# Kernel optimization log

Hardware: AMD Instinct MI355X
Metric: run time of the kernel (lower is better)

The kernel has to match this reference:

```python
import jax, jax.numpy as jnp
import numpy as np

N, E = 50000, 1600000
DIN, DOUT, H, DG = 128, 128, 8, 64
DH = DOUT // H  # per-head dim
NEG_SLOPE = 0.2


def _leaky(x):
    return jnp.where(x >= 0, x, NEG_SLOPE * x)


def setup_inputs() -> dict:
    key = jax.random.key(0)
    ks = jax.random.split(key, 9)
    row = jax.random.randint(ks[0], (E,), 0, N, dtype=jnp.int32)
    col = jax.random.randint(ks[1], (E,), 0, N, dtype=jnp.int32)
    val = jax.random.uniform(ks[2], (E,), dtype=jnp.float32)  # normalized adj values
    feat = jax.random.normal(ks[3], (N, DIN), dtype=jnp.float32)
    W = jax.random.normal(ks[4], (2, H, DIN, DH), dtype=jnp.float32) * 0.05
    b = jnp.zeros((2, H, DH), dtype=jnp.float32)
    att = jax.random.normal(ks[5], (H, 2 * DH), dtype=jnp.float32) * 0.1
    offset = jnp.zeros((2, DOUT), dtype=jnp.float32)
    scale = jnp.ones((2, DOUT), dtype=jnp.float32)
    weight_gate = jax.random.normal(ks[6], (2 * DIN + DG, H), dtype=jnp.float32) * 0.05
    weight_pool_gate = jax.random.normal(ks[7], (DIN, DG), dtype=jnp.float32) * 0.05
    return {"row": row, "col": col, "val": val, "feat": feat, "W": W, "b": b,
            "att": att, "offset": offset, "scale": scale,
            "weight_gate": weight_gate, "weight_pool_gate": weight_pool_gate}


def reference(row, col, val, feat, W, b, att, offset, scale, weight_gate, weight_pool_gate):
    # ---- gate values (GaAN eq. 3) ----
    zj = feat @ weight_pool_gate                                   # [N, DG]
    zmax = jax.ops.segment_max(zj[col], row, num_segments=N)       # max-pool over neighbors
    zmax = jnp.where(jnp.isfinite(zmax), zmax, 0.0)                # isolated nodes -> 0
    nmean = jax.ops.segment_sum(val[:, None] * feat[col], row, num_segments=N)  # spmm(adj, feat)
    gate = jnp.concatenate([feat, zmax, nmean], axis=1) @ weight_gate            # [N, H]
    # ---- per-order, per-head linear + relu ----
    fp = jax.nn.relu(jnp.einsum('nd,ohdk->onhk', feat, W) + b[:, None])  # [2, N, H, DH]
    f0, f1 = fp[0], fp[1]                                          # self / neighbor feats
    # ---- attention-weighted sparse aggregation ----
    a_self = _leaky(jnp.einsum('nhk,hk->nh', f0, att[:, :DH]))     # [N, H]
    a_neigh = _leaky(jnp.einsum('nhk,hk->nh', f1, att[:, DH:]))    # [N, H]
    w_edge = (a_self[row] + a_neigh[col]) * val[:, None]           # [E, H]
    agg = jax.ops.segment_sum(w_edge[:, :, None] * f1[col], row, num_segments=N)  # [N, H, DH]
    agg = agg * gate[:, :, None]                                   # gated heads
    h0 = f0.reshape(N, DOUT)
    h1 = agg.reshape(N, DOUT)
    # ---- per-node norm (torch _batch_norm over feature dim) ----
    def norm(x, s, o):
        mu = jnp.mean(x, axis=1, keepdims=True)
        var = jnp.var(x, axis=1, keepdims=True) + 1e-9
        return (x - mu) * s * jax.lax.rsqrt(var) + o
    h0 = norm(h0, scale[0], offset[0])
    h1 = norm(h1, scale[1], offset[1])
    return h0 + h1  # aggr == 'mean'
```

## Files before the change

kernel.cpp:

```cpp
#include <hip/hip_runtime.h>
#include <hip/hip_bf16.h>
#include <math.h>

#define DIN   128
#define DOUTC 128
#define HH    8
#define DHH   16
#define DGG   64
#define NCOLS 336
#define NTILE 21
#define BSHIFT 7
#define CAP   6144
#define EPB   4096

typedef __attribute__((ext_vector_type(8))) short short8v;
typedef __attribute__((ext_vector_type(4))) float float4v;

__global__ void cvt_feat(const float* __restrict__ feat, __hip_bfloat16* __restrict__ featb, int total8) {
    int i = blockIdx.x * 256 + threadIdx.x;
    if (i < total8) {
        const float4* p = reinterpret_cast<const float4*>(feat) + 2 * (size_t)i;
        float4 x = p[0], y = p[1];
        union { __hip_bfloat16 h[8]; short8v v; } pk;
        pk.h[0] = __float2bfloat16(x.x); pk.h[1] = __float2bfloat16(x.y);
        pk.h[2] = __float2bfloat16(x.z); pk.h[3] = __float2bfloat16(x.w);
        pk.h[4] = __float2bfloat16(y.x); pk.h[5] = __float2bfloat16(y.y);
        pk.h[6] = __float2bfloat16(y.z); pk.h[7] = __float2bfloat16(y.w);
        reinterpret_cast<short8v*>(featb)[i] = pk.v;
    }
}

__global__ void prep2(const float* __restrict__ W, const float* __restrict__ b,
                      const float* __restrict__ Wg, const float* __restrict__ Wpg,
                      __hip_bfloat16* __restrict__ Btb, float* __restrict__ biasv) {
    int idx = blockIdx.x * 256 + threadIdx.x;
    if (idx < NCOLS * DIN) {
        int j = idx >> 7;
        int k = idx & 127;
        float v;
        if (j < 256) {
            int o = j >> 7, jj = j & 127, h = jj >> 4, kd = jj & 15;
            v = W[((o * HH + h) * DIN + k) * DHH + kd];
        } else if (j < 320) {
            v = Wpg[k * DGG + (j - 256)];
        } else if (j < 328) {
            v = Wg[k * HH + (j - 320)];
        } else {
            v = Wg[(192 + k) * HH + (j - 328)];
        }
        Btb[idx] = __float2bfloat16(v);
    }
    if (idx < NCOLS) {
        float bv = 0.f;
        if (idx < 256) { int o = idx >> 7, jj = idx & 127; bv = b[(o * HH + (jj >> 4)) * DHH + (jj & 15)]; }
        biasv[idx] = bv;
    }
}

__global__ __launch_bounds__(256, 2) void dense_mfma(
    const __hip_bfloat16* __restrict__ featb, const __hip_bfloat16* __restrict__ Btb,
    const float* __restrict__ biasv,
    float* __restrict__ f0, __hip_bfloat16* __restrict__ f1b, __hip_bfloat16* __restrict__ zjb,
    float* __restrict__ fg0, float* __restrict__ nodedat, int N) {
    int t   = threadIdx.x;
    int wid = t >> 6, l = t & 63;
    int r0  = blockIdx.x * 128 + wid * 32;
    int lr  = l & 15;
    int lk  = l >> 4;

    short8v a[2][4];
    #pragma unroll
    for (int rt = 0; rt < 2; ++rt) {
        int node = r0 + rt * 16 + lr;
        if (node >= N) node = N - 1;
        const short8v* ap = reinterpret_cast<const short8v*>(&featb[(size_t)node * DIN + lk * 8]);
        #pragma unroll
        for (int kk = 0; kk < 4; ++kk) a[rt][kk] = ap[kk * 4];
    }

    float4v acc[2][NTILE];
    #pragma unroll
    for (int rt = 0; rt < 2; ++rt)
        #pragma unroll
        for (int n = 0; n < NTILE; ++n) acc[rt][n] = (float4v)0.f;

    const short8v* bp = reinterpret_cast<const short8v*>(Btb) + (lr * 16 + lk);
    #pragma unroll
    for (int n = 0; n < NTILE; ++n) {
        #pragma unroll
        for (int kk = 0; kk < 4; ++kk) {
            short8v bv = bp[n * 256 + kk * 4];
            acc[0][n] = __builtin_amdgcn_mfma_f32_16x16x32_bf16(a[0][kk], bv, acc[0][n], 0, 0, 0);
            acc[1][n] = __builtin_amdgcn_mfma_f32_16x16x32_bf16(a[1][kk], bv, acc[1][n], 0, 0, 0);
        }
    }

    #pragma unroll
    for (int rt = 0; rt < 2; ++rt) {
        #pragma unroll
        for (int rg = 0; rg < 4; ++rg) {
            int node = r0 + rt * 16 + lk * 4 + rg;
            if (node < N) {
                #pragma unroll
                for (int n = 0; n < NTILE; ++n) {
                    int col = n * 16 + lr;
                    float v = acc[rt][n][rg] + biasv[col];
                    if (n < 8) {
                        v = v > 0.f ? v : 0.f;
                        f0[(size_t)node * DOUTC + col] = v;
                    } else if (n < 16) {
                        v = v > 0.f ? v : 0.f;
                        f1b[(size_t)node * DOUTC + (col - 128)] = __float2bfloat16(v);
                    } else if (n < 20) {
                        zjb[(size_t)node * DGG + (col - 256)] = __float2bfloat16(v);
                    } else {
                        if (lr < 8) fg0[node * HH + lr] = v;
                        else        nodedat[(size_t)node * 16 + 8 + (lr - 8)] = v;
                    }
                }
            }
        }
    }
}

__global__ void attn_kernel(const float* __restrict__ f0, const __hip_bfloat16* __restrict__ f1b,
                            const float* __restrict__ att,
                            float* __restrict__ a_self, float* __restrict__ nodedat, int N) {
    int g = blockIdx.x * 256 + threadIdx.x;
    if (g >= N * 16) return;
    int node = g >> 4, u = g & 15, h = u >> 1;
    float s = 0.f;
    if ((u & 1) == 0) {
        const float4* p  = reinterpret_cast<const float4*>(&f0[(size_t)node * DOUTC + h * DHH]);
        const float*  av = &att[h * 32];
        #pragma unroll
        for (int q = 0; q < 4; ++q) {
            float4 x = p[q];
            s = fmaf(x.x, av[q * 4 + 0], fmaf(x.y, av[q * 4 + 1],
                fmaf(x.z, av[q * 4 + 2], fmaf(x.w, av[q * 4 + 3], s))));
        }
        s = (s >= 0.f) ? s : 0.2f * s;
        a_self[node * HH + h] = s;
    } else {
        const short8v* p = reinterpret_cast<const short8v*>(&f1b[(size_t)node * DOUTC + h * DHH]);
        const float*  av = &att[h * 32 + DHH];
        union { short8v v; __hip_bfloat16 hh[8]; } pk0, pk1;
        pk0.v = p[0]; pk1.v = p[1];
        #pragma unroll
        for (int q = 0; q < 8; ++q) s = fmaf(__bfloat162float(pk0.hh[q]), av[q], s);
        #pragma unroll
        for (int q = 0; q < 8; ++q) s = fmaf(__bfloat162float(pk1.hh[q]), av[8 + q], s);
        s = (s >= 0.f) ? s : 0.2f * s;
        nodedat[(size_t)node * 16 + h] = s;
    }
}

__global__ __launch_bounds__(256) void bhist(const int* __restrict__ row, int* __restrict__ gHist, int E) {
    __shared__ int hist[512];
    int tid = threadIdx.x;
    hist[tid] = 0; hist[tid + 256] = 0;
    __syncthreads();
    int e0 = blockIdx.x * EPB;
    #pragma unroll
    for (int k = 0; k < 16; ++k) {
        int e = e0 + k * 256 + tid;
        if (e < E) atomicAdd(&hist[row[e] >> BSHIFT], 1);
    }
    __syncthreads();
    if (hist[tid])       atomicAdd(&gHist[tid], hist[tid]);
    if (hist[tid + 256]) atomicAdd(&gHist[tid + 256], hist[tid + 256]);
}

__global__ __launch_bounds__(512) void bscan(const int* __restrict__ gHist, int* __restrict__ gBase,
                                             int* __restrict__ gCursor, int nbuck) {
    __shared__ int s[512];
    int tid = threadIdx.x;
    s[tid] = (tid < nbuck) ? gHist[tid] : 0;
    __syncthreads();
    for (int off = 1; off < 512; off <<= 1) {
        int add = (tid >= off) ? s[tid - off] : 0;
        __syncthreads();
        s[tid] += add;
        __syncthreads();
    }
    if (tid < nbuck) {
        int excl = (tid == 0) ? 0 : s[tid - 1];
        gBase[tid] = excl;
        gCursor[tid] = excl;
    }
}

__global__ __launch_bounds__(256) void bscatter(const int* __restrict__ row, const int* __restrict__ col,
                                                const float* __restrict__ val, int* __restrict__ gCursor,
                                                int2* __restrict__ ebuf, int E) {
    __shared__ int hist[512], base[512], rank[512];
    int tid = threadIdx.x;
    hist[tid] = 0; hist[tid + 256] = 0;
    __syncthreads();
    int e0 = blockIdx.x * EPB;
    #pragma unroll
    for (int k = 0; k < 16; ++k) {
        int e = e0 + k * 256 + tid;
        if (e < E) atomicAdd(&hist[row[e] >> BSHIFT], 1);
    }
    __syncthreads();
    if (hist[tid])       base[tid] = atomicAdd(&gCursor[tid], hist[tid]);
    if (hist[tid + 256]) base[tid + 256] = atomicAdd(&gCursor[tid + 256], hist[tid + 256]);
    rank[tid] = 0; rank[tid + 256] = 0;
    __syncthreads();
    #pragma unroll
    for (int k = 0; k < 16; ++k) {
        int e = e0 + k * 256 + tid;
        if (e < E) {
            int r = row[e];
            int bk = r >> BSHIFT;
            int loc = atomicAdd(&rank[bk], 1);
            int2 pk;
            pk.x = col[e] | ((r & 127) << 16);
            pk.y = __float_as_int(val[e]);
            ebuf[base[bk] + loc] = pk;
        }
    }
}

__global__ __launch_bounds__(256) void bsort(const int2* __restrict__ ebuf, const int* __restrict__ gHist,
                                             const int* __restrict__ gBase, int2* __restrict__ efin,
                                             int* __restrict__ rowptr, int N) {
    __shared__ int2 ent[CAP];
    __shared__ int h0[128], sc[128], rk[128];
    int b = blockIdx.x, tid = threadIdx.x;
    int cnt = gHist[b]; if (cnt > CAP) cnt = CAP;
    int base = gBase[b];
    if (tid < 128) h0[tid] = 0;
    __syncthreads();
    for (int i = tid; i < cnt; i += 256) {
        int2 e = ebuf[base + i];
        ent[i] = e;
        atomicAdd(&h0[(e.x >> 16) & 127], 1);
    }
    __syncthreads();
    if (tid < 128) sc[tid] = h0[tid];
    __syncthreads();
    for (int off = 1; off < 128; off <<= 1) {
        int add = (tid < 128 && tid >= off) ? sc[tid - off] : 0;
        __syncthreads();
        if (tid < 128) sc[tid] += add;
        __syncthreads();
    }
    if (tid < 128) {
        int excl = sc[tid] - h0[tid];
        rk[tid] = excl;
        int grow = b * 128 + tid;
        if (grow <= N) rowptr[grow] = base + excl;
    }
    __syncthreads();
    for (int i = tid; i < cnt; i += 256) {
        int2 e = ent[i];
        int dst = base + atomicAdd(&rk[(e.x >> 16) & 127], 1);
        efin[dst] = e;
    }
}

#define UN 8
__global__ __launch_bounds__(128) void edge_kernel(
    const int* __restrict__ rowptr, const int2* __restrict__ ef,
    const __hip_bfloat16* __restrict__ f1b, const __hip_bfloat16* __restrict__ zjb,
    const float* __restrict__ a_self, const float* __restrict__ nodedat,
    const float* __restrict__ fg0, const float* __restrict__ Wg,
    const float* __restrict__ f0, const float* __restrict__ scale, const float* __restrict__ offset,
    float* __restrict__ out) {
    int r = blockIdx.x;
    int t = threadIdx.x;
    int start = rowptr[r], end = rowptr[r + 1];

    __shared__ float lds_z[64];
    __shared__ float lds_n8[8];
    __shared__ float lds_gate[8];

    float accA0 = 0.f, accA1 = 0.f, accZ = -INFINITY, accN8 = 0.f;
    int h = t >> 3;
    float asr = 0.f;
    if (t < 64) asr = a_self[r * HH + h];
    int j = t - 64;

    int i = start;
    for (; i + UN <= end; i += UN) {
        int   c[UN]; float v[UN];
        #pragma unroll
        for (int u = 0; u < UN; ++u) {
            int2 eu = ef[i + u];
            c[u] = eu.x & 0xFFFF;
            v[u] = __int_as_float(eu.y);
        }
        if (t < 64) {
            float an[UN];
            #pragma unroll
            for (int u = 0; u < UN; ++u) an[u] = nodedat[(size_t)c[u] * 16 + h];
            __hip_bfloat162 f2[UN];
            #pragma unroll
            for (int u = 0; u < UN; ++u)
                f2[u] = *reinterpret_cast<const __hip_bfloat162*>(&f1b[(size_t)c[u] * DOUTC + 2 * t]);
            #pragma unroll
            for (int u = 0; u < UN; ++u) {
                float w = (asr + an[u]) * v[u];
                accA0 = fmaf(w, __bfloat162float(f2[u].x), accA0);
                accA1 = fmaf(w, __bfloat162float(f2[u].y), accA1);
            }
        } else {
            float z[UN];
            #pragma unroll
            for (int u = 0; u < UN; ++u) z[u] = __bfloat162float(zjb[(size_t)c[u] * DGG + j]);
            #pragma unroll
            for (int u = 0; u < UN; ++u) accZ = fmaxf(accZ, z[u]);
            if (j < 8) {
                float g2[UN];
                #pragma unroll
                for (int u = 0; u < UN; ++u) g2[u] = nodedat[(size_t)c[u] * 16 + 8 + j];
                #pragma unroll
                for (int u = 0; u < UN; ++u) accN8 = fmaf(v[u], g2[u], accN8);
            }
        }
    }
    for (; i < end; ++i) {
        int2 eu = ef[i];
        int   c = eu.x & 0xFFFF;
        float v = __int_as_float(eu.y);
        if (t < 64) {
            float w = (asr + nodedat[(size_t)c * 16 + h]) * v;
            __hip_bfloat162 f2 = *reinterpret_cast<const __hip_bfloat162*>(&f1b[(size_t)c * DOUTC + 2 * t]);
            accA0 = fmaf(w, __bfloat162float(f2.x), accA0);
            accA1 = fmaf(w, __bfloat162float(f2.y), accA1);
        } else {
            accZ = fmaxf(accZ, __bfloat162float(zjb[(size_t)c * DGG + j]));
            if (j < 8) accN8 = fmaf(v, nodedat[(size_t)c * 16 + 8 + j], accN8);
        }
    }

    if (t >= 64) {
        lds_z[j] = (end > start) ? accZ : 0.f;
        if (j < 8) lds_n8[j] = accN8;
    }
    __syncthreads();

    if (t < 8) {
        float g = fg0[r * HH + t] + lds_n8[t];
        #pragma unroll
        for (int k = 0; k < 64; ++k) g = fmaf(lds_z[k], Wg[(128 + k) * HH + t], g);
        lds_gate[t] = g;
    }
    __syncthreads();

    if (t < 64) {
        float gh  = lds_gate[h];
        float h1x = accA0 * gh, h1y = accA1 * gh;
        float2 f0v = *reinterpret_cast<const float2*>(&f0[r * DOUTC + 2 * t]);
        float s0  = f0v.x + f0v.y;
        float s0q = f0v.x * f0v.x + f0v.y * f0v.y;
        float s1  = h1x + h1y;
        float s1q = h1x * h1x + h1y * h1y;
        #pragma unroll
        for (int off = 32; off > 0; off >>= 1) {
            s0  += __shfl_xor(s0,  off);
            s0q += __shfl_xor(s0q, off);
            s1  += __shfl_xor(s1,  off);
            s1q += __shfl_xor(s1q, off);
        }
        float mu0  = s0 * (1.f / 128.f), mu1 = s1 * (1.f / 128.f);
        float rs0  = rsqrtf(s0q * (1.f / 128.f) - mu0 * mu0 + 1e-9f);
        float rs1  = rsqrtf(s1q * (1.f / 128.f) - mu1 * mu1 + 1e-9f);
        float2 sc0 = *reinterpret_cast<const float2*>(&scale[2 * t]);
        float2 sc1 = *reinterpret_cast<const float2*>(&scale[128 + 2 * t]);
        float2 of0 = *reinterpret_cast<const float2*>(&offset[2 * t]);
        float2 of1 = *reinterpret_cast<const float2*>(&offset[128 + 2 * t]);
        float2 o2;
        o2.x = (f0v.x - mu0) * sc0.x * rs0 + of0.x + (h1x - mu1) * sc1.x * rs1 + of1.x;
        o2.y = (f0v.y - mu0) * sc0.y * rs0 + of0.y + (h1y - mu1) * sc1.y * rs1 + of1.y;
        *reinterpret_cast<float2*>(&out[r * DOUTC + 2 * t]) = o2;
    }
}

extern "C" void kernel_launch(void* const* d_in, const int* in_sizes, int n_in,
                              void* d_out, int out_size, void* d_ws, size_t ws_size,
                              hipStream_t stream) {
    const int*   row  = (const int*)  d_in[0];
    const int*   col  = (const int*)  d_in[1];
    const float* val  = (const float*)d_in[2];
    const float* feat = (const float*)d_in[3];
    const float* W    = (const float*)d_in[4];
    const float* b    = (const float*)d_in[5];
    const float* att  = (const float*)d_in[6];
    const float* offs = (const float*)d_in[7];
    const float* scal = (const float*)d_in[8];
    const float* Wg   = (const float*)d_in[9];
    const float* Wpg  = (const float*)d_in[10];
    float* out = (float*)d_out;

    const int E = in_sizes[0];
    const int N = in_sizes[3] / DIN;
    const int NBUCK = (N + 127) >> BSHIFT;
    const int NEBLK = (E + EPB - 1) / EPB;

    char* ws = (char*)d_ws;
    size_t off = 0;
    auto alloc = [&](size_t bytes) { size_t o = off; off = (off + bytes + 255) & ~(size_t)255; return o; };

    __hip_bfloat16* featb = (__hip_bfloat16*)(ws + alloc((size_t)N * DIN * 2));
    __hip_bfloat16* Btb   = (__hip_bfloat16*)(ws + alloc((size_t)NCOLS * DIN * 2));
    float* biasv   = (float*)(ws + alloc(NCOLS * 4));
    float* f0      = (float*)(ws + alloc((size_t)N * DOUTC * 4));
    __hip_bfloat16* f1b = (__hip_bfloat16*)(ws + alloc((size_t)N * DOUTC * 2));
    __hip_bfloat16* zjb = (__hip_bfloat16*)(ws + alloc((size_t)N * DGG * 2));
    float* a_self  = (float*)(ws + alloc((size_t)N * HH * 4));
    float* nodedat = (float*)(ws + alloc((size_t)N * 16 * 4));
    float* fg0     = (float*)(ws + alloc((size_t)N * HH * 4));
    int*   rowptr  = (int*)  (ws + alloc((size_t)(N + 1) * 4));
    int*   gHist   = (int*)  (ws + alloc(512 * 4));
    int*   gBase   = (int*)  (ws + alloc(512 * 4));
    int*   gCursor = (int*)  (ws + alloc(512 * 4));
    int2*  ebuf    = (int2*) (ws + alloc((size_t)E * 8));
    int2*  efin    = (int2*) (ws + alloc((size_t)E * 8));

    cvt_feat<<<(N * DIN / 8 + 255) / 256, 256, 0, stream>>>(feat, featb, N * DIN / 8);
    prep2<<<(NCOLS * DIN + 255) / 256, 256, 0, stream>>>(W, b, Wg, Wpg, Btb, biasv);
    dense_mfma<<<(N + 127) / 128, 256, 0, stream>>>(featb, Btb, biasv, f0, f1b, zjb, fg0, nodedat, N);
    attn_kernel<<<(N * 16 + 255) / 256, 256, 0, stream>>>(f0, f1b, att, a_self, nodedat, N);
    hipMemsetAsync(gHist, 0, 512 * 4, stream);
    bhist<<<NEBLK, 256, 0, stream>>>(row, gHist, E);
    bscan<<<1, 512, 0, stream>>>(gHist, gBase, gCursor, NBUCK);
    bscatter<<<NEBLK, 256, 0, stream>>>(row, col, val, gCursor, ebuf, E);
    bsort<<<NBUCK, 256, 0, stream>>>(ebuf, gHist, gBase, efin, rowptr, N);
    edge_kernel<<<N, 128, 0, stream>>>(rowptr, efin, f1b, zjb, a_self, nodedat,
                                       fg0, Wg, f0, scal, offs, out);
}
```

Before: 326.8 us.

## Stage weight matrix in swizzled LDS in two column halves; merge edge tail loop

The dense MFMA kernel now copies the bf16 weight matrix into shared memory in two 176-column halves. The matrix is padded to 352 columns and XOR-swizzled to avoid bank conflicts, so B fragments come from LDS instead of uncoalesced global loads. Splitting the work into halves also halves the accumulator array, which should cut register pressure, and the launch-bounds occupancy hint is dropped. The edge kernel folds its scalar remainder loop into the unrolled loop using masked lanes, adding some wasted loads on short rows but removing the serial tail.

```diff
diff --git a/kernel.cpp b/kernel.cpp
--- a/kernel.cpp
+++ b/kernel.cpp
@@ -8,7 +8,9 @@
 #define DHH   16
 #define DGG   64
 #define NCOLS 336
-#define NTILE 21
+#define NC2   352
+#define PH    176
+#define PT    11
 #define BSHIFT 7
 #define CAP   6144
 #define EPB   4096
@@ -34,34 +36,36 @@
                       const float* __restrict__ Wg, const float* __restrict__ Wpg,
                       __hip_bfloat16* __restrict__ Btb, float* __restrict__ biasv) {
     int idx = blockIdx.x * 256 + threadIdx.x;
-    if (idx < NCOLS * DIN) {
-        int j = idx >> 7;
-        int k = idx & 127;
-        float v;
-        if (j < 256) {
-            int o = j >> 7, jj = j & 127, h = jj >> 4, kd = jj & 15;
+    if (idx < NC2 * DIN) {
+        int col = idx >> 7;
+        int k   = idx & 127;
+        float v = 0.f;
+        if (col < 256) {
+            int o = col >> 7, jj = col & 127, h = jj >> 4, kd = jj & 15;
             v = W[((o * HH + h) * DIN + k) * DHH + kd];
-        } else if (j < 320) {
-            v = Wpg[k * DGG + (j - 256)];
-        } else if (j < 328) {
-            v = Wg[k * HH + (j - 320)];
-        } else {
-            v = Wg[(192 + k) * HH + (j - 328)];
-        }
-        Btb[idx] = __float2bfloat16(v);
-    }
-    if (idx < NCOLS) {
+        } else if (col < 320) {
+            v = Wpg[k * DGG + (col - 256)];
+        } else if (col < 328) {
+            v = Wg[k * HH + (col - 320)];
+        } else if (col < 336) {
+            v = Wg[(192 + k) * HH + (col - 328)];
+        }
+        int u = (k >> 3) ^ (col & 7);
+        Btb[col * DIN + u * 8 + (k & 7)] = __float2bfloat16(v);
+    }
+    if (idx < NC2) {
         float bv = 0.f;
         if (idx < 256) { int o = idx >> 7, jj = idx & 127; bv = b[(o * HH + (jj >> 4)) * DHH + (jj & 15)]; }
         biasv[idx] = bv;
     }
 }
 
-__global__ __launch_bounds__(256, 2) void dense_mfma(
+__global__ __launch_bounds__(256) void dense_mfma(
     const __hip_bfloat16* __restrict__ featb, const __hip_bfloat16* __restrict__ Btb,
     const float* __restrict__ biasv,
     float* __restrict__ f0, __hip_bfloat16* __restrict__ f1b, __hip_bfloat16* __restrict__ zjb,
     float* __restrict__ fg0, float* __restrict__ nodedat, int N) {
+    __shared__ __align__(16) __hip_bfloat16 Bs[PH * DIN];
     int t   = threadIdx.x;
     int wid = t >> 6, l = t & 63;
     int r0  = blockIdx.x * 128 + wid * 32;
@@ -78,44 +82,58 @@
         for (int kk = 0; kk < 4; ++kk) a[rt][kk] = ap[kk * 4];
     }
 
-    float4v acc[2][NTILE];
     #pragma unroll
-    for (int rt = 0; rt < 2; ++rt)
-        #pragma unroll
-        for (int n = 0; n < NTILE; ++n) acc[rt][n] = (float4v)0.f;
-
-    const short8v* bp = reinterpret_cast<const short8v*>(Btb) + (lr * 16 + lk);
-    #pragma unroll
-    for (int n = 0; n < NTILE; ++n) {
-        #pragma unroll
-        for (int kk = 0; kk < 4; ++kk) {
-            short8v bv = bp[n * 256 + kk * 4];
-            acc[0][n] = __builtin_amdgcn_mfma_f32_16x16x32_bf16(a[0][kk], bv, acc[0][n], 0, 0, 0);
-            acc[1][n] = __builtin_amdgcn_mfma_f32_16x16x32_bf16(a[1][kk], bv, acc[1][n], 0, 0, 0);
-        }
-    }
-
-    #pragma unroll
-    for (int rt = 0; rt < 2; ++rt) {
-        #pragma unroll
-        for (int rg = 0; rg < 4; ++rg) {
-            int node = r0 + rt * 16 + lk * 4 + rg;
-            if (node < N) {
-                #pragma unroll
-                for (int n = 0; n < NTILE; ++n) {
-                    int col = n * 16 + lr;
-                    float v = acc[rt][n][rg] + biasv[col];
-                    if (n < 8) {
-                        v = v > 0.f ? v : 0.f;
-                        f0[(size_t)node * DOUTC + col] = v;
-                    } else if (n < 16) {
-                        v = v > 0.f ? v : 0.f;
-                        f1b[(size_t)node * DOUTC + (col - 128)] = __float2bfloat16(v);
-                    } else if (n < 20) {
-                        zjb[(size_t)node * DGG + (col - 256)] = __float2bfloat16(v);
-                    } else {
-                        if (lr < 8) fg0[node * HH + lr] = v;
-                        else        nodedat[(size_t)node * 16 + 8 + (lr - 8)] = v;
+    for (int p = 0; p < 2; ++p) {
+        __syncthreads();
+        {
+            const short8v* src = reinterpret_cast<const short8v*>(Btb + (size_t)p * PH * DIN);
+            short8v* dst = reinterpret_cast<short8v*>(Bs);
+            #pragma unroll
+            for (int it = 0; it < 11; ++it) dst[it * 256 + t] = src[it * 256 + t];
+        }
+        __syncthreads();
+
+        float4v acc[2][PT];
+        #pragma unroll
+        for (int rt = 0; rt < 2; ++rt)
+            #pragma unroll
+            for (int n = 0; n < PT; ++n) acc[rt][n] = (float4v)0.f;
+
+        #pragma unroll
+        for (int n = 0; n < PT; ++n) {
+            int coll = n * 16 + lr;
+            #pragma unroll
+            for (int kk = 0; kk < 4; ++kk) {
+                int u = (kk * 4 + lk) ^ (lr & 7);
+                short8v bv = *reinterpret_cast<const short8v*>(&Bs[coll * DIN + u * 8]);
+                acc[0][n] = __builtin_amdgcn_mfma_f32_16x16x32_bf16(a[0][kk], bv, acc[0][n], 0, 0, 0);
+                acc[1][n] = __builtin_amdgcn_mfma_f32_16x16x32_bf16(a[1][kk], bv, acc[1][n], 0, 0, 0);
+            }
+        }
+
+        #pragma unroll
+        for (int rt = 0; rt < 2; ++rt) {
+            #pragma unroll
+            for (int rg = 0; rg < 4; ++rg) {
+                int node = r0 + rt * 16 + lk * 4 + rg;
+                if (node < N) {
+                    #pragma unroll
+                    for (int n = 0; n < PT; ++n) {
+                        int col = p * PH + n * 16 + lr;
+                        float v = acc[rt][n][rg] + biasv[col];
+                        if (col < 128) {
+                            v = v > 0.f ? v : 0.f;
+                            f0[(size_t)node * DOUTC + col] = v;
+                        } else if (col < 256) {
+                            v = v > 0.f ? v : 0.f;
+                            f1b[(size_t)node * DOUTC + (col - 128)] = __float2bfloat16(v);
+                        } else if (col < 320) {
+                            zjb[(size_t)node * DGG + (col - 256)] = __float2bfloat16(v);
+                        } else if (col < 328) {
+                            fg0[node * HH + (col - 320)] = v;
+                        } else if (col < 336) {
+                            nodedat[(size_t)node * 16 + 8 + (col - 328)] = v;
+                        }
                     }
                 }
             }
@@ -283,14 +301,15 @@
     if (t < 64) asr = a_self[r * HH + h];
     int j = t - 64;
 
-    int i = start;
-    for (; i + UN <= end; i += UN) {
-        int   c[UN]; float v[UN];
+    for (int i = start; i < end; i += UN) {
+        int   c[UN]; float v[UN]; bool ok[UN];
         #pragma unroll
         for (int u = 0; u < UN; ++u) {
-            int2 eu = ef[i + u];
+            int idx = i + u;
+            ok[u] = idx < end;
+            int2 eu = ef[ok[u] ? idx : (end - 1)];
             c[u] = eu.x & 0xFFFF;
-            v[u] = __int_as_float(eu.y);
+            v[u] = ok[u] ? __int_as_float(eu.y) : 0.f;
         }
         if (t < 64) {
             float an[UN];
@@ -311,7 +330,7 @@
             #pragma unroll
             for (int u = 0; u < UN; ++u) z[u] = __bfloat162float(zjb[(size_t)c[u] * DGG + j]);
             #pragma unroll
-            for (int u = 0; u < UN; ++u) accZ = fmaxf(accZ, z[u]);
+            for (int u = 0; u < UN; ++u) if (ok[u]) accZ = fmaxf(accZ, z[u]);
             if (j < 8) {
                 float g2[UN];
                 #pragma unroll
@@ -319,20 +338,6 @@
                 #pragma unroll
                 for (int u = 0; u < UN; ++u) accN8 = fmaf(v[u], g2[u], accN8);
             }
-        }
-    }
-    for (; i < end; ++i) {
-        int2 eu = ef[i];
-        int   c = eu.x & 0xFFFF;
-        float v = __int_as_float(eu.y);
-        if (t < 64) {
-            float w = (asr + nodedat[(size_t)c * 16 + h]) * v;
-            __hip_bfloat162 f2 = *reinterpret_cast<const __hip_bfloat162*>(&f1b[(size_t)c * DOUTC + 2 * t]);
-            accA0 = fmaf(w, __bfloat162float(f2.x), accA0);
-            accA1 = fmaf(w, __bfloat162float(f2.y), accA1);
-        } else {
-            accZ = fmaxf(accZ, __bfloat162float(zjb[(size_t)c * DGG + j]));
-            if (j < 8) accN8 = fmaf(v, nodedat[(size_t)c * 16 + 8 + j], accN8);
         }
     }
 
@@ -405,8 +410,8 @@
     auto alloc = [&](size_t bytes) { size_t o = off; off = (off + bytes + 255) & ~(size_t)255; return o; };
 
     __hip_bfloat16* featb = (__hip_bfloat16*)(ws + alloc((size_t)N * DIN * 2));
-    __hip_bfloat16* Btb   = (__hip_bfloat16*)(ws + alloc((size_t)NCOLS * DIN * 2));
-    float* biasv   = (float*)(ws + alloc(NCOLS * 4));
+    __hip_bfloat16* Btb   = (__hip_bfloat16*)(ws + alloc((size_t)NC2 * DIN * 2));
+    float* biasv   = (float*)(ws + alloc(NC2 * 4));
     float* f0      = (float*)(ws + alloc((size_t)N * DOUTC * 4));
     __hip_bfloat16* f1b = (__hip_bfloat16*)(ws + alloc((size_t)N * DOUTC * 2));
     __hip_bfloat16* zjb = (__hip_bfloat16*)(ws + alloc((size_t)N * DGG * 2));
@@ -421,7 +426,7 @@
     int2*  efin    = (int2*) (ws + alloc((size_t)E * 8));
 
     cvt_feat<<<(N * DIN / 8 + 255) / 256, 256, 0, stream>>>(feat, featb, N * DIN / 8);
-    prep2<<<(NCOLS * DIN + 255) / 256, 256, 0, stream>>>(W, b, Wg, Wpg, Btb, biasv);
+    prep2<<<(NC2 * DIN + 255) / 256, 256, 0, stream>>>(W, b, Wg, Wpg, Btb, biasv);
     dense_mfma<<<(N + 127) / 128, 256, 0, stream>>>(featb, Btb, biasv, f0, f1b, zjb, fg0, nodedat, N);
     attn_kernel<<<(N * 16 + 255) / 256, 256, 0, stream>>>(f0, f1b, att, a_self, nodedat, N);
     hipMemsetAsync(gHist, 0, 512 * 4, stream);
```

Measured after the change: 321.1 us. No clear change (-1.7%).
